# Optimization experiments

Measured on AMD Instinct MI355X. Metric: run time of the kernel, lower is better.

The kernel has to match this reference:

```python
import jax, jax.numpy as jnp
import numpy as np

V, E, H, L = 10000, 50, 100, 5  # vocab, embed_dim, hidden, num_layers
B, T = 32, 512


def setup_inputs() -> dict:
    key = jax.random.key(0)
    ks = jax.random.split(key, 7)
    return {
        "inputs": jax.random.randint(ks[0], (B, T), 0, V),
        "embedding": jax.random.normal(ks[1], (V, E), jnp.float32),
        "Wx0": jax.random.normal(ks[2], (E, 4 * H), jnp.float32) * 0.01,
        "Wh0": jax.random.normal(ks[3], (H, 4 * H), jnp.float32) * 0.01,
        "b0": jnp.zeros((4 * H,), jnp.float32),
        "Wx": jax.random.normal(ks[4], (L - 1, H, 4 * H), jnp.float32) * 0.01,
        "Wh": jax.random.normal(ks[5], (L - 1, H, 4 * H), jnp.float32) * 0.01,
        "b": jnp.zeros((L - 1, 4 * H), jnp.float32),
        "fc_w": jax.random.normal(ks[6], (H, V), jnp.float32) * 0.01,
        "fc_b": jnp.zeros((V,), jnp.float32),
    }


def _cell(x, h, c, Wx_l, Wh_l, b_l):
    # gates concatenated in order (i, f, o, c_tilde)
    g = x @ Wx_l + h @ Wh_l + b_l  # [B, 4H]
    i, f, o, ct = jnp.split(g, 4, axis=-1)
    c_new = jax.nn.sigmoid(f) * c + jax.nn.sigmoid(i) * jnp.tanh(ct)
    h_new = jax.nn.sigmoid(o) * jnp.tanh(c_new)
    return h_new, c_new


def reference(inputs, embedding, Wx0, Wh0, b0, Wx, Wh, b, fc_w, fc_b):
    Bsz, Tlen = inputs.shape
    Hd = Wh0.shape[0]
    nL = Wh.shape[0] + 1
    dt = embedding.dtype
    h0 = jnp.zeros((nL, Bsz, Hd), dt)
    c0 = jnp.zeros((nL, Bsz, Hd), dt)

    def step(carry, tok):
        h, c = carry
        x = embedding[tok]  # [B, E]
        hs, cs = [], []
        hn, cn = _cell(x, h[0], c[0], Wx0, Wh0, b0)
        hs.append(hn); cs.append(cn)
        inp = hn
        for l in range(nL - 1):  # fixed small layer count
            hn, cn = _cell(inp, h[l + 1], c[l + 1], Wx[l], Wh[l], b[l])
            hs.append(hn); cs.append(cn)
            inp = hn
        y = inp @ fc_w + fc_b  # [B, V]
        return (jnp.stack(hs), jnp.stack(cs)), y

    (_, _), ys = jax.lax.scan(step, (h0, c0), inputs.T)  # ys: [T, B, V]
    return jnp.transpose(ys, (1, 0, 2))  # [B, T, V]
```

## Files before the change

### kernel.cpp

```cpp
#include <hip/hip_runtime.h>
#include <cmath>

#define TT 512
#define BB 32
#define HH 100
#define EE 50
#define NL 5
#define VV 10000
#define CCH 8
#define PROGSTR 16

__device__ __forceinline__ float sigmf(float x) { return 1.f / (1.f + __expf(-x)); }

__device__ __forceinline__ void waitge(int* p, int target) {
    int spins = 0;
    while (__hip_atomic_load(p, __ATOMIC_ACQUIRE, __HIP_MEMORY_SCOPE_AGENT) < target) {
        if (++spins > 30000000) break;
    }
}

__global__ __launch_bounds__(256, 1) void lstm_rec2(
    const int* __restrict__ toks, const float* __restrict__ emb,
    const float* __restrict__ Wx0, const float* __restrict__ Wh0, const float* __restrict__ b0,
    const float* __restrict__ WxU, const float* __restrict__ WhU, const float* __restrict__ bU,
    float* __restrict__ ring, float* __restrict__ h4, int* __restrict__ prog, int RS)
{
    const int l = blockIdx.x >> 5;
    const int b = blockIdx.x & 31;
    const int tid = threadIdx.x;
    const int j = tid >> 1;
    const int kh = tid & 1;
    const bool act = (tid < 2 * HH);
    const int jc = (j < HH) ? j : HH - 1;

    __shared__ __align__(16) float vbuf[2][224];

    const float* WxL = (l == 0) ? Wx0 : WxU + (size_t)(l - 1) * (HH * 400);
    const float* WhL = (l == 0) ? Wh0 : WhU + (size_t)(l - 1) * (HH * 400);
    const float* bL  = (l == 0) ? b0  : bU  + (size_t)(l - 1) * 400;

    float W[4][HH];
    float bias[4];
    #pragma unroll
    for (int g = 0; g < 4; ++g) {
        const int c = g * HH + jc;
        bias[g] = bL[c];
        if (kh == 0) {
            #pragma unroll
            for (int kk = 0; kk < HH; ++kk) {
                float v = 0.f;
                if (l != 0 || kk < EE) v = WxL[kk * 400 + c];
                W[g][kk] = v;
            }
        } else {
            #pragma unroll
            for (int kk = 0; kk < HH; ++kk) W[g][kk] = WhL[kk * 400 + c];
        }
    }

    const int ringstr = RS * CCH * HH;
    const int rsm = RS - 1;
    int* progSelf = prog + (l * 32 + b) * PROGSTR;
    int* progDown = prog + ((l - 1) * 32 + b) * PROGSTR;
    int* progUp   = prog + ((l + 1) * 32 + b) * PROGSTR;
    const float* ringDown = ring + (size_t)((l - 1) * 32 + b) * ringstr;
    float*       ringSelf = ring + (size_t)(l * 32 + b) * ringstr;
    float*       h4b      = h4 + (size_t)b * HH;

    if (tid < HH) vbuf[0][HH + tid] = 0.f;
    if (l > 0) {
        if (tid == 0) waitge(progDown, 1);
        __syncthreads();
        if (tid < HH) vbuf[0][tid] = ringDown[tid];
    } else {
        if (tid < HH) {
            float xv = 0.f;
            if (tid < EE) { int tok = toks[b * TT]; xv = emb[(size_t)tok * EE + tid]; }
            vbuf[0][tid] = xv;
        }
    }
    __syncthreads();

    float cstate = 0.f;

    for (int t = 0; t < TT; ++t) {
        const int p = t & 1;
        if (tid == 0) {
            if ((t & 7) == 0 && l < NL - 1) {
                int e = t >> 3;
                if (e >= RS) waitge(progUp, e - RS + 1);
            }
            if (((t + 1) & 7) == 0 && (t + 1) < TT && l > 0)
                waitge(progDown, ((t + 1) >> 3) + 1);
        }
        __syncthreads();

        const int tn = t + 1;
        float xp = 0.f;
        if (act && kh == 1 && tn < TT) {
            if (l == 0) {
                if (j < EE) { int tok = toks[b * TT + tn]; xp = emb[(size_t)tok * EE + j]; }
            } else {
                xp = ringDown[(size_t)((((tn >> 3) & rsm) * CCH) + (tn & 7)) * HH + j];
            }
        }

        float acc[4] = {0.f, 0.f, 0.f, 0.f};
        const float* vb = &vbuf[p][kh * HH];
        #pragma unroll
        for (int kk = 0; kk < 25; ++kk) {
            const float4 vv = *reinterpret_cast<const float4*>(vb + 4 * kk);
            #pragma unroll
            for (int g = 0; g < 4; ++g) {
                acc[g] = fmaf(vv.x, W[g][4 * kk + 0], acc[g]);
                acc[g] = fmaf(vv.y, W[g][4 * kk + 1], acc[g]);
                acc[g] = fmaf(vv.z, W[g][4 * kk + 2], acc[g]);
                acc[g] = fmaf(vv.w, W[g][4 * kk + 3], acc[g]);
            }
        }
        #pragma unroll
        for (int g = 0; g < 4; ++g) acc[g] += __shfl_xor(acc[g], 1);

        if (act) {
            if (kh == 0) {
                float gi = acc[0] + bias[0], gf = acc[1] + bias[1];
                float go = acc[2] + bias[2], gc = acc[3] + bias[3];
                float cn = sigmf(gf) * cstate + sigmf(gi) * tanhf(gc);
                cstate = cn;
                float hn = sigmf(go) * tanhf(cn);
                vbuf[p ^ 1][HH + j] = hn;
                if (l == NL - 1) h4b[(size_t)t * (BB * HH) + j] = hn;
                else ringSelf[(size_t)((((t >> 3) & rsm) * CCH) + (t & 7)) * HH + j] = hn;
            } else {
                vbuf[p ^ 1][j] = xp;
            }
        }

        if ((t & 7) == 7) {
            __syncthreads();
            __threadfence();
            if (tid == 0)
                __hip_atomic_store(progSelf, (t >> 3) + 1, __ATOMIC_RELEASE,
                                   __HIP_MEMORY_SCOPE_AGENT);
        }
    }
}

__global__ __launch_bounds__(256) void fc2(
    const float* __restrict__ h4, const float* __restrict__ fcw,
    const float* __restrict__ fcb, float* __restrict__ out)
{
    const int v0 = blockIdx.x * 128;
    const int R0 = blockIdx.y * 128;
    const int tid = threadIdx.x;
    const int tv = tid & 15, tr = tid >> 4;
    __shared__ __align__(16) float As[HH][132];
    __shared__ __align__(16) float Bs[HH][132];
    const int b = R0 >> 9;
    const int t0 = R0 & 511;

    for (int idx = tid; idx < 128 * HH; idx += 256) {
        int r = idx / HH, k = idx - r * HH;
        As[k][r] = h4[(size_t)(t0 + r) * (BB * HH) + b * HH + k];
    }
    for (int idx = tid; idx < HH * 128; idx += 256) {
        int k = idx >> 7, vl = idx & 127;
        int v = v0 + vl;
        Bs[k][vl] = (v < VV) ? fcw[(size_t)k * VV + v] : 0.f;
    }
    __syncthreads();

    float acc[8][8];
    #pragma unroll
    for (int i = 0; i < 8; ++i)
        #pragma unroll
        for (int q = 0; q < 8; ++q) acc[i][q] = 0.f;

    for (int k = 0; k < HH; ++k) {
        const float4 aL = *reinterpret_cast<const float4*>(&As[k][4 * tr]);
        const float4 aH = *reinterpret_cast<const float4*>(&As[k][64 + 4 * tr]);
        const float4 bL = *reinterpret_cast<const float4*>(&Bs[k][4 * tv]);
        const float4 bH = *reinterpret_cast<const float4*>(&Bs[k][64 + 4 * tv]);
        const float a[8] = {aL.x, aL.y, aL.z, aL.w, aH.x, aH.y, aH.z, aH.w};
        const float bb[8] = {bL.x, bL.y, bL.z, bL.w, bH.x, bH.y, bH.z, bH.w};
        #pragma unroll
        for (int i = 0; i < 8; ++i)
            #pragma unroll
            for (int q = 0; q < 8; ++q)
                acc[i][q] = fmaf(a[i], bb[q], acc[i][q]);
    }

    #pragma unroll
    for (int i = 0; i < 8; ++i) {
        const int r = R0 + 64 * (i >> 2) + 4 * tr + (i & 3);
        float* orow = out + (size_t)r * VV;
        #pragma unroll
        for (int ch = 0; ch < 2; ++ch) {
            const int v = v0 + 64 * ch + 4 * tv;
            if (v + 3 < VV) {
                float4 o;
                o.x = acc[i][4 * ch + 0] + fcb[v + 0];
                o.y = acc[i][4 * ch + 1] + fcb[v + 1];
                o.z = acc[i][4 * ch + 2] + fcb[v + 2];
                o.w = acc[i][4 * ch + 3] + fcb[v + 3];
                *reinterpret_cast<float4*>(orow + v) = o;
            } else {
                #pragma unroll
                for (int q = 0; q < 4; ++q)
                    if (v + q < VV) orow[v + q] = acc[i][4 * ch + q] + fcb[v + q];
            }
        }
    }
}

extern "C" void kernel_launch(void* const* d_in, const int* in_sizes, int n_in,
                              void* d_out, int out_size, void* d_ws, size_t ws_size,
                              hipStream_t stream)
{
    const int*   toks = (const int*)d_in[0];
    const float* emb  = (const float*)d_in[1];
    const float* Wx0  = (const float*)d_in[2];
    const float* Wh0  = (const float*)d_in[3];
    const float* b0   = (const float*)d_in[4];
    const float* WxU  = (const float*)d_in[5];
    const float* WhU  = (const float*)d_in[6];
    const float* bU   = (const float*)d_in[7];
    const float* fcw  = (const float*)d_in[8];
    const float* fcb  = (const float*)d_in[9];
    float* out = (float*)d_out;

    char* ws = (char*)d_ws;
    int* prog = (int*)ws;
    const size_t h4_bytes = (size_t)TT * BB * HH * 4;
    const size_t ring4 = (size_t)4 * 32 * 4 * CCH * HH * 4;
    int RS = (ws_size >= 16384 + ring4 + h4_bytes) ? 4 : 2;
    float* ring = (float*)(ws + 16384);
    float* h4   = (float*)(ws + 16384 + (size_t)4 * 32 * RS * CCH * HH * 4);

    hipMemsetAsync(ws, 0, 16384, stream);
    lstm_rec2<<<NL * 32, 256, 0, stream>>>(toks, emb, Wx0, Wh0, b0,
                                           WxU, WhU, bU, ring, h4, prog, RS);
    fc2<<<dim3((VV + 127) / 128, (BB * TT) / 128), 256, 0, stream>>>(h4, fcw, fcb, out);
}
```

Measured before the change: 3.475 ms.

## Split LSTM gates across four lanes per unit and shrink FC row tile

The recurrent kernel now uses 512 threads per block, with four lanes per hidden unit. Each lane holds two gates' weights for one input half, so register pressure drops from 400 to 200 floats per thread. The gate nonlinearities are computed in parallel across lanes and combined with shuffles, shortening the serial per-step critical path. The FC kernel halves its row tile to 64 so more blocks launch, and it loads the weight tile with float4 vector loads. The cost is more threads and shuffles per step in the recurrence and lower per-thread reuse in the FC GEMM.

```diff
diff --git a/kernel.cpp b/kernel.cpp
--- a/kernel.cpp
+++ b/kernel.cpp
@@ -19,7 +19,7 @@
     }
 }
 
-__global__ __launch_bounds__(256, 1) void lstm_rec2(
+__global__ __launch_bounds__(512, 2) void lstm_rec3(
     const int* __restrict__ toks, const float* __restrict__ emb,
     const float* __restrict__ Wx0, const float* __restrict__ Wh0, const float* __restrict__ b0,
     const float* __restrict__ WxU, const float* __restrict__ WhU, const float* __restrict__ bU,
@@ -28,35 +28,34 @@
     const int l = blockIdx.x >> 5;
     const int b = blockIdx.x & 31;
     const int tid = threadIdx.x;
-    const int j = tid >> 1;
-    const int kh = tid & 1;
-    const bool act = (tid < 2 * HH);
-    const int jc = (j < HH) ? j : HH - 1;
-
-    __shared__ __align__(16) float vbuf[2][224];
+    const int j = tid >> 2;
+    const int s = tid & 3;
+    const int khalf = s & 1;
+    const int gp = s >> 1;
+    const bool act = (j < HH);
+    const int jc = act ? j : HH - 1;
+
+    __shared__ __align__(16) float vbuf[2][208];
 
     const float* WxL = (l == 0) ? Wx0 : WxU + (size_t)(l - 1) * (HH * 400);
     const float* WhL = (l == 0) ? Wh0 : WhU + (size_t)(l - 1) * (HH * 400);
     const float* bL  = (l == 0) ? b0  : bU  + (size_t)(l - 1) * 400;
 
-    float W[4][HH];
-    float bias[4];
-    #pragma unroll
-    for (int g = 0; g < 4; ++g) {
-        const int c = g * HH + jc;
-        bias[g] = bL[c];
-        if (kh == 0) {
+    float W[2][HH];
+    {
+        const float* Wsrc = khalf ? WhL : WxL;
+        #pragma unroll
+        for (int gg = 0; gg < 2; ++gg) {
+            const int c = (2 * gp + gg) * HH + jc;
             #pragma unroll
             for (int kk = 0; kk < HH; ++kk) {
-                float v = 0.f;
-                if (l != 0 || kk < EE) v = WxL[kk * 400 + c];
-                W[g][kk] = v;
-            }
-        } else {
-            #pragma unroll
-            for (int kk = 0; kk < HH; ++kk) W[g][kk] = WhL[kk * 400 + c];
-        }
-    }
+                float w = 0.f;
+                if (khalf == 1 || l != 0 || kk < EE) w = Wsrc[kk * 400 + c];
+                W[gg][kk] = w;
+            }
+        }
+    }
+    const float biasv = bL[s * HH + jc];
 
     const int ringstr = RS * CCH * HH;
     const int rsm = RS - 1;
@@ -66,6 +65,7 @@
     const float* ringDown = ring + (size_t)((l - 1) * 32 + b) * ringstr;
     float*       ringSelf = ring + (size_t)(l * 32 + b) * ringstr;
     float*       h4b      = h4 + (size_t)b * HH;
+    const int*   tokb     = toks + b * TT;
 
     if (tid < HH) vbuf[0][HH + tid] = 0.f;
     if (l > 0) {
@@ -75,7 +75,7 @@
     } else {
         if (tid < HH) {
             float xv = 0.f;
-            if (tid < EE) { int tok = toks[b * TT]; xv = emb[(size_t)tok * EE + tid]; }
+            if (tid < EE) { int tok = tokb[0]; xv = emb[(size_t)tok * EE + tid]; }
             vbuf[0][tid] = xv;
         }
     }
@@ -97,41 +97,46 @@
 
         const int tn = t + 1;
         float xp = 0.f;
-        if (act && kh == 1 && tn < TT) {
+        if (act && s == 1 && tn < TT) {
             if (l == 0) {
-                if (j < EE) { int tok = toks[b * TT + tn]; xp = emb[(size_t)tok * EE + j]; }
+                if (j < EE) { int tok = tokb[tn]; xp = emb[(size_t)tok * EE + j]; }
             } else {
                 xp = ringDown[(size_t)((((tn >> 3) & rsm) * CCH) + (tn & 7)) * HH + j];
             }
         }
 
-        float acc[4] = {0.f, 0.f, 0.f, 0.f};
-        const float* vb = &vbuf[p][kh * HH];
+        float acc0 = 0.f, acc1 = 0.f;
+        const float* vb = &vbuf[p][khalf * HH];
         #pragma unroll
         for (int kk = 0; kk < 25; ++kk) {
             const float4 vv = *reinterpret_cast<const float4*>(vb + 4 * kk);
-            #pragma unroll
-            for (int g = 0; g < 4; ++g) {
-                acc[g] = fmaf(vv.x, W[g][4 * kk + 0], acc[g]);
-                acc[g] = fmaf(vv.y, W[g][4 * kk + 1], acc[g]);
-                acc[g] = fmaf(vv.z, W[g][4 * kk + 2], acc[g]);
-                acc[g] = fmaf(vv.w, W[g][4 * kk + 3], acc[g]);
-            }
-        }
-        #pragma unroll
-        for (int g = 0; g < 4; ++g) acc[g] += __shfl_xor(acc[g], 1);
+            acc0 = fmaf(vv.x, W[0][4 * kk + 0], acc0);
+            acc0 = fmaf(vv.y, W[0][4 * kk + 1], acc0);
+            acc0 = fmaf(vv.z, W[0][4 * kk + 2], acc0);
+            acc0 = fmaf(vv.w, W[0][4 * kk + 3], acc0);
+            acc1 = fmaf(vv.x, W[1][4 * kk + 0], acc1);
+            acc1 = fmaf(vv.y, W[1][4 * kk + 1], acc1);
+            acc1 = fmaf(vv.z, W[1][4 * kk + 2], acc1);
+            acc1 = fmaf(vv.w, W[1][4 * kk + 3], acc1);
+        }
+        acc0 += __shfl_xor(acc0, 1);
+        acc1 += __shfl_xor(acc1, 1);
+
+        float g = ((s & 1) ? acc1 : acc0) + biasv;
+        float es = (s == 3) ? tanhf(g) : sigmf(g);
+        float f1 = __shfl_xor(es, 1);
+        float f2 = __shfl_xor(es, 2);
+        float f3 = __shfl_xor(es, 3);
 
         if (act) {
-            if (kh == 0) {
-                float gi = acc[0] + bias[0], gf = acc[1] + bias[1];
-                float go = acc[2] + bias[2], gc = acc[3] + bias[3];
-                float cn = sigmf(gf) * cstate + sigmf(gi) * tanhf(gc);
+            if (s == 0) {
+                float cn = f1 * cstate + es * f3;
                 cstate = cn;
-                float hn = sigmf(go) * tanhf(cn);
+                float hn = f2 * tanhf(cn);
                 vbuf[p ^ 1][HH + j] = hn;
                 if (l == NL - 1) h4b[(size_t)t * (BB * HH) + j] = hn;
                 else ringSelf[(size_t)((((t >> 3) & rsm) * CCH) + (t & 7)) * HH + j] = hn;
-            } else {
+            } else if (s == 1) {
                 vbuf[p ^ 1][j] = xp;
             }
         }
@@ -146,53 +151,61 @@
     }
 }
 
-__global__ __launch_bounds__(256) void fc2(
+__global__ __launch_bounds__(256) void fc3(
     const float* __restrict__ h4, const float* __restrict__ fcw,
     const float* __restrict__ fcb, float* __restrict__ out)
 {
     const int v0 = blockIdx.x * 128;
-    const int R0 = blockIdx.y * 128;
+    const int R0 = blockIdx.y * 64;
     const int tid = threadIdx.x;
     const int tv = tid & 15, tr = tid >> 4;
-    __shared__ __align__(16) float As[HH][132];
+    __shared__ __align__(16) float As[HH][68];
     __shared__ __align__(16) float Bs[HH][132];
     const int b = R0 >> 9;
     const int t0 = R0 & 511;
 
-    for (int idx = tid; idx < 128 * HH; idx += 256) {
-        int r = idx / HH, k = idx - r * HH;
-        As[k][r] = h4[(size_t)(t0 + r) * (BB * HH) + b * HH + k];
-    }
-    for (int idx = tid; idx < HH * 128; idx += 256) {
-        int k = idx >> 7, vl = idx & 127;
-        int v = v0 + vl;
-        Bs[k][vl] = (v < VV) ? fcw[(size_t)k * VV + v] : 0.f;
+    for (int idx = tid; idx < 64 * HH; idx += 256) {
+        int rr = idx / HH, kk = idx - rr * HH;
+        As[kk][rr] = h4[(size_t)(t0 + rr) * (BB * HH) + b * HH + kk];
+    }
+    for (int i4 = tid; i4 < HH * 32; i4 += 256) {
+        int k = i4 >> 5, m = i4 & 31;
+        int v = v0 + 4 * m;
+        float4 w;
+        if (v + 3 < VV) {
+            w = *reinterpret_cast<const float4*>(fcw + (size_t)k * VV + v);
+        } else {
+            w.x = (v + 0 < VV) ? fcw[(size_t)k * VV + v + 0] : 0.f;
+            w.y = (v + 1 < VV) ? fcw[(size_t)k * VV + v + 1] : 0.f;
+            w.z = (v + 2 < VV) ? fcw[(size_t)k * VV + v + 2] : 0.f;
+            w.w = (v + 3 < VV) ? fcw[(size_t)k * VV + v + 3] : 0.f;
+        }
+        *reinterpret_cast<float4*>(&Bs[k][4 * m]) = w;
     }
     __syncthreads();
 
-    float acc[8][8];
+    float acc[4][8];
     #pragma unroll
-    for (int i = 0; i < 8; ++i)
+    for (int i = 0; i < 4; ++i)
         #pragma unroll
         for (int q = 0; q < 8; ++q) acc[i][q] = 0.f;
 
     for (int k = 0; k < HH; ++k) {
-        const float4 aL = *reinterpret_cast<const float4*>(&As[k][4 * tr]);
-        const float4 aH = *reinterpret_cast<const float4*>(&As[k][64 + 4 * tr]);
+        const float4 a4 = *reinterpret_cast<const float4*>(&As[k][4 * tr]);
         const float4 bL = *reinterpret_cast<const float4*>(&Bs[k][4 * tv]);
         const float4 bH = *reinterpret_cast<const float4*>(&Bs[k][64 + 4 * tv]);
-        const float a[8] = {aL.x, aL.y, aL.z, aL.w, aH.x, aH.y, aH.z, aH.w};
+        const float a[4] = {a4.x, a4.y, a4.z, a4.w};
         const float bb[8] = {bL.x, bL.y, bL.z, bL.w, bH.x, bH.y, bH.z, bH.w};
         #pragma unroll
-        for (int i = 0; i < 8; ++i)
+        for (int i = 0; i < 4; ++i)
             #pragma unroll
             for (int q = 0; q < 8; ++q)
                 acc[i][q] = fmaf(a[i], bb[q], acc[i][q]);
     }
 
     #pragma unroll
-    for (int i = 0; i < 8; ++i) {
-        const int r = R0 + 64 * (i >> 2) + 4 * tr + (i & 3);
+    for (int i = 0; i < 4; ++i) {
+        const int r = R0 + 4 * tr + i;
         float* orow = out + (size_t)r * VV;
         #pragma unroll
         for (int ch = 0; ch < 2; ++ch) {
@@ -238,7 +251,7 @@
     float* h4   = (float*)(ws + 16384 + (size_t)4 * 32 * RS * CCH * HH * 4);
 
     hipMemsetAsync(ws, 0, 16384, stream);
-    lstm_rec2<<<NL * 32, 256, 0, stream>>>(toks, emb, Wx0, Wh0, b0,
+    lstm_rec3<<<NL * 32, 512, 0, stream>>>(toks, emb, Wx0, Wh0, b0,
                                            WxU, WhU, bU, ring, h4, prog, RS);
-    fc2<<<dim3((VV + 127) / 128, (BB * TT) / 128), 256, 0, stream>>>(h4, fcw, fcb, out);
-}
+    fc3<<<dim3((VV + 127) / 128, (BB * TT) / 64), 256, 0, stream>>>(h4, fcw, fcb, out);
+}
```

After: 3.466 ms. About the same (-0.3%).
